# Performance work log

Hardware: AMD Instinct MI355X
Metric: run time of the kernel (lower is better)

Reference implementation:

```python
import jax, jax.numpy as jnp
import numpy as np

NUM_HEADS = 16
EMBED_DIM = 1024
INPUT_DIM = 1024
B, S = 4, 1024
MASK_VAL = -1e30  # fp32 branch of the original code


def setup_inputs() -> dict:
    key = jax.random.key(0)
    k1, k2, k3, k4 = jax.random.split(key, 4)
    x = jax.random.normal(k1, (B, S, INPUT_DIM), dtype=jnp.float32)
    mask = jax.random.randint(k2, (B, S), 0, 2, dtype=jnp.int32)
    # xavier_uniform-like init
    lim_qkv = float(np.sqrt(6.0 / (INPUT_DIM + 3 * EMBED_DIM)))
    lim_out = float(np.sqrt(6.0 / (EMBED_DIM + EMBED_DIM)))
    w_qkv = jax.random.uniform(k3, (3 * EMBED_DIM, INPUT_DIM), jnp.float32, -lim_qkv, lim_qkv)
    b_qkv = jnp.zeros((3 * EMBED_DIM,), jnp.float32)
    w_out = jax.random.uniform(k4, (EMBED_DIM, EMBED_DIM), jnp.float32, -lim_out, lim_out)
    b_out = jnp.zeros((EMBED_DIM,), jnp.float32)
    return {"x": x, "mask": mask, "w_qkv": w_qkv, "b_qkv": b_qkv,
            "w_out": w_out, "b_out": b_out}


def reference(x, mask, w_qkv, b_qkv, w_out, b_out):
    Bz, Sl, _ = x.shape
    Dh = EMBED_DIM // NUM_HEADS
    qkv = x @ w_qkv.T + b_qkv                       # (B,S,3E)
    q, k, v = jnp.split(qkv, 3, axis=-1)
    q = q.reshape(Bz, Sl, NUM_HEADS, Dh).transpose(0, 2, 1, 3)  # (B,H,S,Dh)
    k = k.reshape(Bz, Sl, NUM_HEADS, Dh).transpose(0, 2, 1, 3)
    v = v.reshape(Bz, Sl, NUM_HEADS, Dh).transpose(0, 2, 1, 3)
    energy = jnp.einsum('bhqd,bhkd->bhqk', q, k) / jnp.sqrt(jnp.float32(Dh))
    # Faithful reproduction of the original (buggy-looking) mask semantics:
    # positions with (k <= q) & (q < L_i) & (k < L_i) get filled with -1e30.
    L = mask.sum(axis=-1)                            # (B,)
    idx = jnp.arange(Sl)
    tri = idx[:, None] >= idx[None, :]               # (S,S): k <= q
    valid = idx[None, :] < L[:, None]                # (B,S)
    cond = tri[None, None] & valid[:, None, :, None] & valid[:, None, None, :]
    energy = jnp.where(cond, MASK_VAL, energy)
    attn = jax.nn.softmax(energy, axis=-1)           # (B,H,S,S)
    out = jnp.einsum('bhqk,bhkd->bhqd', attn, v)     # (B,H,S,Dh)
    out = out.transpose(0, 2, 1, 3).reshape(Bz, Sl, EMBED_DIM)
    return out @ w_out.T + b_out
```

## Files before the change

### kernel.cpp

```cpp
#include <hip/hip_runtime.h>


#define NHEADS 16
#define DHEAD  64
#define EDIM   1024
#define SLEN   1024
#define BATCH  4

typedef short bf16x8 __attribute__((ext_vector_type(8)));
typedef float f32x4  __attribute__((ext_vector_type(4)));
typedef float f32x16 __attribute__((ext_vector_type(16)));

#define MFMA_BF16(a,b,c) __builtin_amdgcn_mfma_f32_16x16x32_bf16((a),(b),(c),0,0,0)
#define MFMA32(a,b,c)    __builtin_amdgcn_mfma_f32_32x32x16_bf16((a),(b),(c),0,0,0)

typedef const __attribute__((address_space(1))) void gvoid_t;
typedef __attribute__((address_space(3))) void lvoid_t;

__device__ __forceinline__ unsigned short f2bf(float x) {
  union { float f; unsigned int u; } v; v.f = x;
  unsigned int r = v.u + 0x7fffu + ((v.u >> 16) & 1u);
  return (unsigned short)(r >> 16);
}

__device__ __forceinline__ unsigned pack2(float lo, float hi) {
  return (unsigned)f2bf(lo) | ((unsigned)f2bf(hi) << 16);
}

__device__ __forceinline__ void gl2lds16(const void* g, void* l) {
  __builtin_amdgcn_global_load_lds((gvoid_t*)g, (lvoid_t*)l, 16, 0, 0);
}

__global__ __launch_bounds__(256) void prep_cast(
    const float* __restrict__ x, const float* __restrict__ wq,
    const float* __restrict__ wo,
    unsigned short* __restrict__ xb, unsigned short* __restrict__ wqb,
    unsigned short* __restrict__ wob) {
  int i = blockIdx.x * 256 + threadIdx.x;
  const int NX  = BATCH * SLEN * EDIM / 4;
  const int NW1 = 3 * EDIM * EDIM / 4;
  const float4* src; unsigned short* dst; int j;
  if (i < NX)           { src = (const float4*)x;  dst = xb;  j = i; }
  else if (i < NX+NW1)  { src = (const float4*)wq; dst = wqb; j = i - NX; }
  else                  { src = (const float4*)wo; dst = wob; j = i - NX - NW1; }
  float4 v = src[j];
  ushort4 o;
  o.x = f2bf(v.x); o.y = f2bf(v.y); o.z = f2bf(v.z); o.w = f2bf(v.w);
  ((ushort4*)dst)[j] = o;
}

__global__ __launch_bounds__(256) void mask_sum(const int* __restrict__ mask,
                                                int* __restrict__ L) {
  int b = blockIdx.x;
  int t = threadIdx.x;
  int s = 0;
  for (int i = t; i < SLEN; i += 256) s += mask[b * SLEN + i];
  #pragma unroll
  for (int m = 1; m < 64; m <<= 1) s += __shfl_xor(s, m);
  __shared__ int part[4];
  if ((t & 63) == 0) part[t >> 6] = s;
  __syncthreads();
  if (t == 0) L[b] = part[0] + part[1] + part[2] + part[3];
}

template<int EPI>
__global__ __launch_bounds__(256) void gemm_bt(
    const unsigned short* __restrict__ A, const unsigned short* __restrict__ B,
    int M, int N, int K,
    const float* __restrict__ bias,
    float* __restrict__ outf,
    unsigned short* __restrict__ qb, unsigned short* __restrict__ kb,
    unsigned short* __restrict__ vb) {
  __shared__ __align__(16) unsigned short lds_a[128 * 32];
  __shared__ __align__(16) unsigned short lds_b[128 * 32];
  const int tid = threadIdx.x;
  const int w = tid >> 6, l = tid & 63;
  const int g = l >> 4, ln = l & 15;
  const int ntile = N >> 7;
  const int tm = blockIdx.x / ntile, tn = blockIdx.x % ntile;
  const int mBase = tm << 7, nBase = tn << 7;
  const int wr = w >> 1, wc = w & 1;

  f32x4 zz = {0.f, 0.f, 0.f, 0.f};
  f32x4 acc[4][4];
  #pragma unroll
  for (int m = 0; m < 4; ++m)
    #pragma unroll
    for (int n = 0; n < 4; ++n) acc[m][n] = zz;

  const int u0 = tid, u1 = tid + 256;
  const int r0 = u0 >> 2, c0 = (u0 & 3) << 3;
  const int r1 = u1 >> 2, c1 = (u1 & 3) << 3;
  const unsigned short* Ab = A + mBase * K;
  const unsigned short* Bb = B + nBase * K;
  unsigned short* da0 = &lds_a[(w * 64) * 8];
  unsigned short* da1 = &lds_a[(256 + w * 64) * 8];
  unsigned short* db0 = &lds_b[(w * 64) * 8];
  unsigned short* db1 = &lds_b[(256 + w * 64) * 8];

  for (int k0 = 0; k0 < K; k0 += 32) {
    gl2lds16(Ab + r0 * K + k0 + c0, da0);
    gl2lds16(Ab + r1 * K + k0 + c1, da1);
    gl2lds16(Bb + r0 * K + k0 + c0, db0);
    gl2lds16(Bb + r1 * K + k0 + c1, db1);
    __syncthreads();
    bf16x8 af[4], bfr[4];
    #pragma unroll
    for (int m = 0; m < 4; ++m)
      af[m] = *(const bf16x8*)&lds_a[(wr * 64 + m * 16 + ln) * 32 + g * 8];
    #pragma unroll
    for (int n = 0; n < 4; ++n)
      bfr[n] = *(const bf16x8*)&lds_b[(wc * 64 + n * 16 + ln) * 32 + g * 8];
    #pragma unroll
    for (int m = 0; m < 4; ++m)
      #pragma unroll
      for (int n = 0; n < 4; ++n)
        acc[m][n] = MFMA_BF16(af[m], bfr[n], acc[m][n]);
    __syncthreads();
  }

  #pragma unroll
  for (int m = 0; m < 4; ++m) {
    const int rowb = mBase + wr * 64 + m * 16 + g * 4;
    #pragma unroll
    for (int n = 0; n < 4; ++n) {
      const int col = nBase + wc * 64 + n * 16 + ln;
      const float bv = bias[col];
      #pragma unroll
      for (int r = 0; r < 4; ++r) {
        const float vv = acc[m][n][r] + bv;
        const int row = rowb + r;
        if (EPI == 0) {
          const int part = col >> 10;
          const int c = col & 1023;
          const int hh = c >> 6, d = c & 63;
          const int bb = row >> 10, s = row & 1023;
          const int bh = bb * NHEADS + hh;
          const unsigned short hv = f2bf(vv);
          if (part == 0)      qb[(bh * SLEN + s) * DHEAD + d] = hv;
          else if (part == 1) kb[(bh * SLEN + s) * DHEAD + d] = hv;
          else                vb[(bh * DHEAD + d) * SLEN + s] = hv;
        } else {
          outf[row * N + col] = vv;
        }
      }
    }
  }
}

__global__ __launch_bounds__(64) void attn(
    const unsigned short* __restrict__ qb, const unsigned short* __restrict__ kb,
    const unsigned short* __restrict__ vb, const int* __restrict__ Lp,
    unsigned short* __restrict__ yb) {
  const int bid = blockIdx.x;
  const int lid = (bid & 7) * 256 + (bid >> 3);
  const int bh = lid >> 5, qw = lid & 31;
  const int b = bh >> 4, h = bh & 15;
  const int L = Lp[b];
  const int l = threadIdx.x;
  const int l31 = l & 31, hi = l >> 5;
  const int q = qw * 32 + l31;

  const unsigned short* qp = qb + (size_t)bh * SLEN * DHEAD;
  const unsigned short* kp = kb + (size_t)bh * SLEN * DHEAD;
  const unsigned short* vp = vb + (size_t)bh * DHEAD * SLEN;

  bf16x8 qf[4];
  #pragma unroll
  for (int c = 0; c < 4; ++c)
    qf[c] = *(const bf16x8*)&qp[q * DHEAD + c * 16 + hi * 8];

  f32x16 o0 = {}; f32x16 o1 = {};
  float mrow = -__builtin_inff(), lrow = 0.f;
  const bool qv = q < L;

  for (int t = 0; t < SLEN / 32; ++t) {
    const int kb0 = t * 32;
    f32x16 e = {};
    __builtin_amdgcn_s_setprio(1);
    #pragma unroll
    for (int c = 0; c < 4; ++c) {
      const bf16x8 kf = *(const bf16x8*)&kp[(kb0 + l31) * DHEAD + c * 16 + hi * 8];
      e = MFMA32(kf, qf[c], e);
    }
    __builtin_amdgcn_s_setprio(0);

    float pm = -__builtin_inff();
    #pragma unroll
    for (int r = 0; r < 16; ++r) {
      const int key = kb0 + (r & 3) + 8 * (r >> 2) + 4 * hi;
      float s = e[r] * 0.125f;
      if (qv && (key <= q) && (key < L)) s = -1e30f;
      e[r] = s;
      pm = fmaxf(pm, s);
    }
    pm = fmaxf(pm, __shfl_xor(pm, 32));
    const float mn = fmaxf(mrow, pm);
    const float a = __expf(mrow - mn);
    float sum = 0.f;
    #pragma unroll
    for (int r = 0; r < 16; ++r) { const float pe = __expf(e[r] - mn); e[r] = pe; sum += pe; }
    sum += __shfl_xor(sum, 32);
    lrow = lrow * a + sum;
    mrow = mn;
    #pragma unroll
    for (int r = 0; r < 16; ++r) { o0[r] *= a; o1[r] *= a; }

    bf16x8 pbf[2];
    #pragma unroll
    for (int kc = 0; kc < 2; ++kc) {
      const unsigned wA = pack2(e[8*kc+0], e[8*kc+1]);
      const unsigned wB = pack2(e[8*kc+2], e[8*kc+3]);
      const unsigned wC = pack2(e[8*kc+4], e[8*kc+5]);
      const unsigned wD = pack2(e[8*kc+6], e[8*kc+7]);
      const unsigned pA = __shfl_xor(wA, 32);
      const unsigned pB = __shfl_xor(wB, 32);
      const unsigned pC = __shfl_xor(wC, 32);
      const unsigned pD = __shfl_xor(wD, 32);
      union { unsigned u[4]; bf16x8 v; } pk;
      pk.u[0] = hi ? pC : wA;
      pk.u[1] = hi ? pD : wB;
      pk.u[2] = hi ? wC : pA;
      pk.u[3] = hi ? wD : pB;
      pbf[kc] = pk.v;
    }

    __builtin_amdgcn_s_setprio(1);
    #pragma unroll
    for (int kc = 0; kc < 2; ++kc) {
      const bf16x8 vf0 = *(const bf16x8*)&vp[l31 * SLEN + kb0 + kc * 16 + hi * 8];
      const bf16x8 vf1 = *(const bf16x8*)&vp[(32 + l31) * SLEN + kb0 + kc * 16 + hi * 8];
      o0 = MFMA32(vf0, pbf[kc], o0);
      o1 = MFMA32(vf1, pbf[kc], o1);
    }
    __builtin_amdgcn_s_setprio(0);
  }

  const float inv = 1.0f / lrow;
  unsigned short* yrow = yb + (size_t)(b * SLEN + q) * EDIM + h * DHEAD;
  #pragma unroll
  for (int rq = 0; rq < 4; ++rq) {
    ushort4 s0, s1;
    s0.x = f2bf(o0[4*rq+0] * inv); s0.y = f2bf(o0[4*rq+1] * inv);
    s0.z = f2bf(o0[4*rq+2] * inv); s0.w = f2bf(o0[4*rq+3] * inv);
    s1.x = f2bf(o1[4*rq+0] * inv); s1.y = f2bf(o1[4*rq+1] * inv);
    s1.z = f2bf(o1[4*rq+2] * inv); s1.w = f2bf(o1[4*rq+3] * inv);
    *(ushort4*)&yrow[8*rq + 4*hi]      = s0;
    *(ushort4*)&yrow[32 + 8*rq + 4*hi] = s1;
  }
}

extern "C" void kernel_launch(void* const* d_in, const int* in_sizes, int n_in,
                              void* d_out, int out_size, void* d_ws, size_t ws_size,
                              hipStream_t stream) {
  const float* x    = (const float*)d_in[0];
  const int*   mask = (const int*)d_in[1];
  const float* wqkv = (const float*)d_in[2];
  const float* bqkv = (const float*)d_in[3];
  const float* wout = (const float*)d_in[4];
  const float* bout = (const float*)d_in[5];
  float* out = (float*)d_out;

  char* ws = (char*)d_ws;
  const size_t SZ_X   = (size_t)BATCH * SLEN * EDIM * 2;
  const size_t SZ_WQ  = (size_t)3 * EDIM * EDIM * 2;
  const size_t SZ_WO  = (size_t)EDIM * EDIM * 2;
  const size_t SZ_QKV = (size_t)BATCH * NHEADS * SLEN * DHEAD * 2;

  unsigned short* xb   = (unsigned short*)ws;               ws += SZ_X;
  unsigned short* wqb  = (unsigned short*)ws;               ws += SZ_WQ;
  unsigned short* wob  = (unsigned short*)ws;               ws += SZ_WO;
  unsigned short* qbuf = (unsigned short*)ws;               ws += SZ_QKV;
  unsigned short* kbuf = (unsigned short*)ws;               ws += SZ_QKV;
  unsigned short* vbuf = (unsigned short*)ws;               ws += SZ_QKV;
  unsigned short* ybuf = (unsigned short*)ws;               ws += SZ_X;
  int* Lbuf = (int*)ws;

  prep_cast<<<8192, 256, 0, stream>>>(x, wqkv, wout, xb, wqb, wob);
  mask_sum<<<BATCH, 256, 0, stream>>>(mask, Lbuf);
  gemm_bt<0><<<(4096 / 128) * (3072 / 128), 256, 0, stream>>>(
      xb, wqb, 4096, 3072, 1024, bqkv, nullptr, qbuf, kbuf, vbuf);
  attn<<<BATCH * NHEADS * (SLEN / 32), 64, 0, stream>>>(qbuf, kbuf, vbuf, Lbuf, ybuf);
  gemm_bt<1><<<(4096 / 128) * (1024 / 128), 256, 0, stream>>>(
      ybuf, wob, 4096, 1024, 1024, bout, out, nullptr, nullptr, nullptr);
}
```

Measured before the change: 241.1 us.

## Split attention key loop across two waves and skip fully masked key tiles

The attention kernel now runs two waves per block. Each wave handles alternate 32-key tiles, and the two partial softmax states are merged through shared memory at the end. Key tiles that are entirely masked, for query blocks whose rows all fall inside L, are skipped. The softmax now works in the exp2 domain with a folded scale constant and rescales lazily, only when the running max grows by more than a threshold. This cuts per-wave serial work and exp calls, at the cost of an LDS reduction, a barrier, and reliance on the exact mask structure for skipping.

```diff
diff --git a/kernel.cpp b/kernel.cpp
--- a/kernel.cpp
+++ b/kernel.cpp
@@ -148,7 +148,7 @@
   }
 }
 
-__global__ __launch_bounds__(64) void attn(
+__global__ __launch_bounds__(128) void attn(
     const unsigned short* __restrict__ qb, const unsigned short* __restrict__ kb,
     const unsigned short* __restrict__ vb, const int* __restrict__ Lp,
     unsigned short* __restrict__ yb) {
@@ -157,7 +157,8 @@
   const int bh = lid >> 5, qw = lid & 31;
   const int b = bh >> 4, h = bh & 15;
   const int L = Lp[b];
-  const int l = threadIdx.x;
+  const int tid = threadIdx.x;
+  const int w = tid >> 6, l = tid & 63;
   const int l31 = l & 31, hi = l >> 5;
   const int q = qw * 32 + l31;
 
@@ -173,8 +174,14 @@
   f32x16 o0 = {}; f32x16 o1 = {};
   float mrow = -__builtin_inff(), lrow = 0.f;
   const bool qv = q < L;
-
-  for (int t = 0; t < SLEN / 32; ++t) {
+  const float C = 0.18033688011112042f;
+
+  const bool allQ   = (qw * 32 + 31) < L;
+  const bool noneQ  = (qw * 32) >= L;
+  const bool skipOK = allQ && (L < SLEN);
+
+  for (int t = w; t < 32; t += 2) {
+    if (skipOK && t < qw) continue;
     const int kb0 = t * 32;
     f32x16 e = {};
     __builtin_amdgcn_s_setprio(1);
@@ -185,26 +192,44 @@
     }
     __builtin_amdgcn_s_setprio(0);
 
+    const bool domask = (!noneQ) && (t <= qw);
     float pm = -__builtin_inff();
+    if (domask) {
+      #pragma unroll
+      for (int r = 0; r < 16; ++r) {
+        const int key = kb0 + (r & 3) + 8 * (r >> 2) + 4 * hi;
+        float s = e[r] * C;
+        if (qv && (key <= q)) s = -1e30f;
+        e[r] = s;
+        pm = fmaxf(pm, s);
+      }
+    } else {
+      #pragma unroll
+      for (int r = 0; r < 16; ++r) {
+        const float s = e[r] * C;
+        e[r] = s;
+        pm = fmaxf(pm, s);
+      }
+    }
+    pm = fmaxf(pm, __shfl_xor(pm, 32));
+
+    const bool need = !__all(pm <= mrow + 8.0f);
+    if (need) {
+      const float mn = fmaxf(mrow, pm);
+      const float a = exp2f(mrow - mn);
+      #pragma unroll
+      for (int r = 0; r < 16; ++r) { o0[r] *= a; o1[r] *= a; }
+      lrow *= a;
+      mrow = mn;
+    }
+    float sum = 0.f;
     #pragma unroll
     for (int r = 0; r < 16; ++r) {
-      const int key = kb0 + (r & 3) + 8 * (r >> 2) + 4 * hi;
-      float s = e[r] * 0.125f;
-      if (qv && (key <= q) && (key < L)) s = -1e30f;
-      e[r] = s;
-      pm = fmaxf(pm, s);
-    }
-    pm = fmaxf(pm, __shfl_xor(pm, 32));
-    const float mn = fmaxf(mrow, pm);
-    const float a = __expf(mrow - mn);
-    float sum = 0.f;
-    #pragma unroll
-    for (int r = 0; r < 16; ++r) { const float pe = __expf(e[r] - mn); e[r] = pe; sum += pe; }
+      const float pe = exp2f(e[r] - mrow);
+      e[r] = pe; sum += pe;
+    }
     sum += __shfl_xor(sum, 32);
-    lrow = lrow * a + sum;
-    mrow = mn;
-    #pragma unroll
-    for (int r = 0; r < 16; ++r) { o0[r] *= a; o1[r] *= a; }
+    lrow += sum;
 
     bf16x8 pbf[2];
     #pragma unroll
@@ -236,17 +261,43 @@
     __builtin_amdgcn_s_setprio(0);
   }
 
-  const float inv = 1.0f / lrow;
+  __shared__ float ml[2][2][32];
+  __shared__ __align__(16) float obuf[64][34];
+  if (hi == 0) { ml[w][0][l31] = mrow; ml[w][1][l31] = lrow; }
+  if (w == 0) {
+    #pragma unroll
+    for (int r = 0; r < 16; ++r) obuf[l][16 + r] = o1[r];
+  } else {
+    #pragma unroll
+    for (int r = 0; r < 16; ++r) obuf[l][r] = o0[r];
+  }
+  __syncthreads();
+  const float m0 = ml[0][0][l31], m1 = ml[1][0][l31];
+  const float l0 = ml[0][1][l31], l1 = ml[1][1][l31];
+  const float mn = fmaxf(m0, m1);
+  const float s0 = exp2f(m0 - mn), s1 = exp2f(m1 - mn);
+  const float inv = 1.0f / (l0 * s0 + l1 * s1);
   unsigned short* yrow = yb + (size_t)(b * SLEN + q) * EDIM + h * DHEAD;
-  #pragma unroll
-  for (int rq = 0; rq < 4; ++rq) {
-    ushort4 s0, s1;
-    s0.x = f2bf(o0[4*rq+0] * inv); s0.y = f2bf(o0[4*rq+1] * inv);
-    s0.z = f2bf(o0[4*rq+2] * inv); s0.w = f2bf(o0[4*rq+3] * inv);
-    s1.x = f2bf(o1[4*rq+0] * inv); s1.y = f2bf(o1[4*rq+1] * inv);
-    s1.z = f2bf(o1[4*rq+2] * inv); s1.w = f2bf(o1[4*rq+3] * inv);
-    *(ushort4*)&yrow[8*rq + 4*hi]      = s0;
-    *(ushort4*)&yrow[32 + 8*rq + 4*hi] = s1;
+  if (w == 0) {
+    #pragma unroll
+    for (int rq = 0; rq < 4; ++rq) {
+      ushort4 st;
+      st.x = f2bf((o0[4*rq+0] * s0 + obuf[l][4*rq+0] * s1) * inv);
+      st.y = f2bf((o0[4*rq+1] * s0 + obuf[l][4*rq+1] * s1) * inv);
+      st.z = f2bf((o0[4*rq+2] * s0 + obuf[l][4*rq+2] * s1) * inv);
+      st.w = f2bf((o0[4*rq+3] * s0 + obuf[l][4*rq+3] * s1) * inv);
+      *(ushort4*)&yrow[8*rq + 4*hi] = st;
+    }
+  } else {
+    #pragma unroll
+    for (int rq = 0; rq < 4; ++rq) {
+      ushort4 st;
+      st.x = f2bf((obuf[l][16+4*rq+0] * s0 + o1[4*rq+0] * s1) * inv);
+      st.y = f2bf((obuf[l][16+4*rq+1] * s0 + o1[4*rq+1] * s1) * inv);
+      st.z = f2bf((obuf[l][16+4*rq+2] * s0 + o1[4*rq+2] * s1) * inv);
+      st.w = f2bf((obuf[l][16+4*rq+3] * s0 + o1[4*rq+3] * s1) * inv);
+      *(ushort4*)&yrow[32 + 8*rq + 4*hi] = st;
+    }
   }
 }
 
@@ -280,7 +331,7 @@
   mask_sum<<<BATCH, 256, 0, stream>>>(mask, Lbuf);
   gemm_bt<0><<<(4096 / 128) * (3072 / 128), 256, 0, stream>>>(
       xb, wqb, 4096, 3072, 1024, bqkv, nullptr, qbuf, kbuf, vbuf);
-  attn<<<BATCH * NHEADS * (SLEN / 32), 64, 0, stream>>>(qbuf, kbuf, vbuf, Lbuf, ybuf);
+  attn<<<BATCH * NHEADS * (SLEN / 32), 128, 0, stream>>>(qbuf, kbuf, vbuf, Lbuf, ybuf);
   gemm_bt<1><<<(4096 / 128) * (1024 / 128), 256, 0, stream>>>(
       ybuf, wob, 4096, 1024, 1024, bout, out, nullptr, nullptr, nullptr);
 }
```

Result: no change. 244.9 us (+1.6%).
